# Performance work log

Hardware: AMD Instinct MI355X
Metric: run time of the kernel (lower is better)

Reference implementation:

```python
import jax, jax.numpy as jnp
import numpy as np

N = 8192
HID = 256
NCLS = 5
K = 10  # adj_parameter
IN_DIMS = [1000, 1000, 503]


def _leaky(x):
    return jnp.where(x >= 0, x, 0.25 * x)


def _batchnorm(x, g, b):
    # training-mode BatchNorm1d with batch stats (biased var), eps=1e-5
    mu = jnp.mean(x, axis=0)
    var = jnp.mean((x - mu) ** 2, axis=0)
    return (x - mu) * jax.lax.rsqrt(var + 1e-5) * g + b


def _build_adj(feat):
    # cosine similarity, per-row top-(K+1) (top-1 is self, diag=1), scatter,
    # add identity, L1 row-normalize. Vectorized equivalent of the torch loop.
    norm = jnp.maximum(jnp.linalg.norm(feat, axis=1, keepdims=True), 1e-12)
    fn = feat / norm
    sim = fn @ fn.T                                  # [N, N]
    vals, idx = jax.lax.top_k(sim, K + 1)            # [N, K+1]
    rows = jnp.arange(sim.shape[0])[:, None]
    adj = jnp.zeros_like(sim).at[rows, idx[:, 1:]].set(vals[:, 1:])
    adj = adj + jnp.eye(sim.shape[0], dtype=sim.dtype)
    rs = jnp.maximum(jnp.sum(jnp.abs(adj), axis=1, keepdims=True), 1e-12)
    return adj / rs


def setup_inputs() -> dict:
    key = jax.random.key(0)
    ks = jax.random.split(key, 24)
    d = {}
    d['x1'] = jax.random.normal(ks[0], (N, IN_DIMS[0]), jnp.float32)
    d['x2'] = jax.random.normal(ks[1], (N, IN_DIMS[1]), jnp.float32)
    d['x3'] = jax.random.normal(ks[2], (N, IN_DIMS[2]), jnp.float32)
    def xavier(k, shape):
        fan_in, fan_out = shape[-2], shape[-1]
        std = np.sqrt(2.0 / (fan_in + fan_out))
        return jax.random.normal(k, shape, jnp.float32) * std
    d['enc_W1'] = xavier(ks[3], (IN_DIMS[0], HID))
    d['enc_W2'] = xavier(ks[4], (IN_DIMS[1], HID))
    d['enc_W3'] = xavier(ks[5], (IN_DIMS[2], HID))
    d['enc_b'] = jnp.zeros((3, HID), jnp.float32)
    d['bn_g'] = jnp.ones((3, HID), jnp.float32)
    d['bn_b'] = jnp.zeros((3, HID), jnp.float32)
    d['gc1_W'] = xavier(ks[6], (3, HID, HID))
    d['gc1_b'] = jnp.zeros((3, HID), jnp.float32)
    d['gc2_W'] = xavier(ks[7], (3, HID, HID))
    d['gc2_b'] = jnp.zeros((3, HID), jnp.float32)
    d['clf_W'] = xavier(ks[8], (3, HID, NCLS))
    d['clf_b'] = jnp.zeros((3, NCLS), jnp.float32)
    d['attn'] = xavier(ks[9], (3, 1))[:, 0]
    d['f1_W'] = xavier(ks[10], (NCLS, 128))
    d['f1_b'] = jnp.zeros((128,), jnp.float32)
    d['f2_W'] = xavier(ks[11], (128, NCLS))
    d['f2_b'] = jnp.zeros((NCLS,), jnp.float32)
    return d


def reference(x1, x2, x3, enc_W1, enc_W2, enc_W3, enc_b, bn_g, bn_b,
              gc1_W, gc1_b, gc2_W, gc2_b, clf_W, clf_b,
              attn, f1_W, f1_b, f2_W, f2_b):
    xs = [x1, x2, x3]
    enc_Ws = [enc_W1, enc_W2, enc_W3]
    logits_list = []
    for i in range(3):
        # modal encoder: Linear -> ReLU -> BatchNorm (dropout off, eval)
        feat = jax.nn.relu(xs[i] @ enc_Ws[i] + enc_b[i])
        feat = _batchnorm(feat, bn_g[i], bn_b[i])
        adj = _build_adj(feat)
        # SimpleGCN: two GraphConvolution layers with leaky_relu(0.25)
        h = _leaky(adj @ (feat @ gc1_W[i]) + gc1_b[i])
        h = _leaky(adj @ (h @ gc2_W[i]) + gc2_b[i])
        logits_list.append(h @ clf_W[i] + clf_b[i])
    # SimpleVCDN fusion
    w = jax.nn.softmax(attn)
    fused = sum(w[i] * jax.nn.sigmoid(logits_list[i]) for i in range(3))
    out = _leaky(fused @ f1_W + f1_b) @ f2_W + f2_b
    return out
```

## Files before the change

### kernel.cpp

```cpp
#include <hip/hip_runtime.h>
#include <cfloat>
#include <cstdint>
#include <cstddef>

#define NROWS 8192
#define HID 256
#define NCLS 5
#define TOPK 10
#define CAP 256
#define TM 128
#define TN 128
#define BK 32
#define BKS 64

typedef __bf16 bf16x8 __attribute__((ext_vector_type(8)));
typedef float f32x4 __attribute__((ext_vector_type(4)));

__device__ inline ushort f2bf(float x) {
  unsigned u = __float_as_uint(x);
  unsigned r = (u + 0x7fffu + ((u >> 16) & 1u)) >> 16;
  return (ushort)r;
}
__device__ inline float bf2f(ushort b) { return __uint_as_float(((unsigned)b) << 16); }

__device__ __forceinline__ void load_lds16(const void* g, void* l) {
  __builtin_amdgcn_global_load_lds(
      (const __attribute__((address_space(1))) void*)g,
      (__attribute__((address_space(3))) void*)l, 16, 0, 0);
}

__global__ __launch_bounds__(256) void packAB_kernel(const float* __restrict__ X0,
    const float* __restrict__ X1, const float* __restrict__ X2,
    const float* __restrict__ W0, const float* __restrict__ W1,
    const float* __restrict__ W2, ushort* __restrict__ Ah, ushort* __restrict__ Al,
    ushort* __restrict__ Bh, ushort* __restrict__ Bl,
    int D0, int D1, int D2, int Kp0, int Kp1, int Kp2,
    size_t aOff0, size_t aOff1, size_t aOff2,
    size_t wOff0, size_t wOff1, size_t wOff2) {
  const int z = blockIdx.y;
  const float* X = (z == 0) ? X0 : (z == 1) ? X1 : X2;
  const float* W = (z == 0) ? W0 : (z == 1) ? W1 : W2;
  const int D = (z == 0) ? D0 : (z == 1) ? D1 : D2;
  const int Kp = (z == 0) ? Kp0 : (z == 1) ? Kp1 : Kp2;
  const size_t aOff = (z == 0) ? aOff0 : (z == 1) ? aOff1 : aOff2;
  const size_t wOff = (z == 0) ? wOff0 : (z == 1) ? wOff1 : wOff2;
  const int ksh = 31 - __clz(Kp);
  const int id = blockIdx.x * 256 + threadIdx.x;
  const int atotal = NROWS << ksh;
  if (id >= atotal + (HID << ksh)) return;
  if (id < atotal) {
    const int k = id & (Kp - 1);
    const int r = id >> ksh;
    const float x = (k < D) ? X[(size_t)r * D + k] : 0.f;
    const ushort h = f2bf(x);
    Ah[aOff + id] = h;
    Al[aOff + id] = f2bf(x - bf2f(h));
  } else {
    const int id2 = id - atotal;
    const int k = id2 & (Kp - 1);
    const int n = id2 >> ksh;
    const float x = (k < D) ? W[(size_t)k * HID + n] : 0.f;
    const ushort h = f2bf(x);
    Bh[wOff + id2] = h;
    Bl[wOff + id2] = f2bf(x - bf2f(h));
  }
}

__global__ __launch_bounds__(256) void packW_kernel(const float* __restrict__ W,
    ushort* __restrict__ Bh, ushort* __restrict__ Bl) {
  const int z = blockIdx.y;
  const int id = blockIdx.x * 256 + threadIdx.x;
  const int k = id >> 8, n = id & 255;
  const size_t wz = (size_t)z * HID * HID;
  const float x = W[wz + (size_t)k * HID + n];
  const ushort h = f2bf(x);
  Bh[wz + (size_t)n * HID + k] = h;
  Bl[wz + (size_t)n * HID + k] = f2bf(x - bf2f(h));
}

#define STAGE_LIMB(B, K0)                              \
    load_lds16(Ah + a0 + (K0), &AsH[B][p0 * 8]);       \
    load_lds16(Ah + a1 + (K0), &AsH[B][p1 * 8]);       \
    load_lds16(Al + a0 + (K0), &AsL[B][p0 * 8]);       \
    load_lds16(Al + a1 + (K0), &AsL[B][p1 * 8]);       \
    load_lds16(Bh + b0 + (K0), &BsH[B][p0 * 8]);       \
    load_lds16(Bh + b1 + (K0), &BsH[B][p1 * 8]);       \
    load_lds16(Bl + b0 + (K0), &BsL[B][p0 * 8]);       \
    load_lds16(Bl + b1 + (K0), &BsL[B][p1 * 8]);

template<bool BIAS, int ACT>
__global__ __launch_bounds__(256) void limbgemm_kernel(const ushort* __restrict__ Ah,
    const ushort* __restrict__ Al, const ushort* __restrict__ Bh,
    const ushort* __restrict__ Bl, const float* __restrict__ bias,
    float* __restrict__ C, int Kp0, int Kp1, int Kp2,
    size_t aOff0, size_t aOff1, size_t aOff2,
    size_t bOff0, size_t bOff1, size_t bOff2) {
  __shared__ ushort AsH[2][TM * BK], AsL[2][TM * BK], BsH[2][TM * BK], BsL[2][TM * BK];
  const int z = blockIdx.y;
  const int Kp = (z == 0) ? Kp0 : (z == 1) ? Kp1 : Kp2;
  const size_t aO = (z == 0) ? aOff0 : (z == 1) ? aOff1 : aOff2;
  const size_t bO = (z == 0) ? bOff0 : (z == 1) ? bOff1 : bOff2;
  Ah += aO; Al += aO; Bh += bO; Bl += bO;
  C += (size_t)z * NROWS * HID;
  const int tid = threadIdx.x;
  const int wave = tid >> 6, lane = tid & 63;
  const int bid = blockIdx.x;
  const int xcd = bid & 7, slot = bid >> 3;
  const int bxi = slot & 1;
  const int byi = xcd * 8 + (slot >> 1);
  const int bm = byi * TM, bn = bxi * 128;
  const int wr = (wave >> 1) * 64, wc = (wave & 1) * 64;

  f32x4 acc[4][4];
  const f32x4 zero = {0.f, 0.f, 0.f, 0.f};
  #pragma unroll
  for (int i = 0; i < 4; ++i)
    #pragma unroll
    for (int j = 0; j < 4; ++j) acc[i][j] = zero;

  const int p0 = tid, p1 = tid + 256;
  const int r0 = p0 >> 2, kl0 = (p0 & 3) ^ ((r0 & 3) ^ ((r0 >> 2) & 1));
  const int r1 = p1 >> 2, kl1 = (p1 & 3) ^ ((r1 & 3) ^ ((r1 >> 2) & 1));
  const size_t a0 = (size_t)(bm + r0) * Kp + kl0 * 8;
  const size_t a1 = (size_t)(bm + r1) * Kp + kl1 * 8;
  const size_t b0 = (size_t)(bn + r0) * Kp + kl0 * 8;
  const size_t b1 = (size_t)(bn + r1) * Kp + kl1 * 8;

  STAGE_LIMB(0, 0)
  __syncthreads();
  int cur = 0;
  for (int k0 = 0; k0 < Kp; k0 += BK) {
    if (k0 + BK < Kp) {
      STAGE_LIMB(cur ^ 1, k0 + BK)
    }
    bf16x8 ah[4], al[4], bh[4], bl[4];
    const int kg = lane >> 4;
    #pragma unroll
    for (int f = 0; f < 4; ++f) {
      const int m = wr + f * 16 + (lane & 15);
      const int sa = m * 4 + (kg ^ (m & 3) ^ ((m >> 2) & 1));
      ah[f] = *(const bf16x8*)&AsH[cur][sa * 8];
      al[f] = *(const bf16x8*)&AsL[cur][sa * 8];
      const int n = wc + f * 16 + (lane & 15);
      const int sb = n * 4 + (kg ^ (n & 3) ^ ((n >> 2) & 1));
      bh[f] = *(const bf16x8*)&BsH[cur][sb * 8];
      bl[f] = *(const bf16x8*)&BsL[cur][sb * 8];
    }
    #pragma unroll
    for (int fr = 0; fr < 4; ++fr)
      #pragma unroll
      for (int fc = 0; fc < 4; ++fc) {
        acc[fr][fc] = __builtin_amdgcn_mfma_f32_16x16x32_bf16(ah[fr], bh[fc], acc[fr][fc], 0, 0, 0);
        acc[fr][fc] = __builtin_amdgcn_mfma_f32_16x16x32_bf16(ah[fr], bl[fc], acc[fr][fc], 0, 0, 0);
        acc[fr][fc] = __builtin_amdgcn_mfma_f32_16x16x32_bf16(al[fr], bh[fc], acc[fr][fc], 0, 0, 0);
      }
    __syncthreads();
    cur ^= 1;
  }
  const int cq = lane >> 4, cc = lane & 15;
  #pragma unroll
  for (int fr = 0; fr < 4; ++fr) {
    #pragma unroll
    for (int fc = 0; fc < 4; ++fc) {
      const int rb = bm + wr + fr * 16 + cq * 4;
      const int col = bn + wc + fc * 16 + cc;
      const float bb = BIAS ? bias[z * HID + col] : 0.f;
      float* cp = C + (size_t)rb * HID + col;
      #pragma unroll
      for (int e = 0; e < 4; ++e) {
        float v = acc[fr][fc][e] + bb;
        if (ACT == 1) v = fmaxf(v, 0.f);
        cp[(size_t)e * HID] = v;
      }
    }
  }
}

__global__ __launch_bounds__(256) void bn_stats_kernel(const float* __restrict__ F,
    float* __restrict__ ps, float* __restrict__ ps2) {
  const int z = blockIdx.y;
  const int b = blockIdx.x, t = threadIdx.x;
  float s = 0.f, s2 = 0.f;
  const float* p = F + (size_t)z * NROWS * HID + (size_t)b * 128 * HID + t;
  for (int r = 0; r < 128; ++r) {
    const float v = p[(size_t)r * HID];
    s += v; s2 += v * v;
  }
  ps[(size_t)z * 64 * HID + b * HID + t] = s;
  ps2[(size_t)z * 64 * HID + b * HID + t] = s2;
}

__global__ __launch_bounds__(256) void bn_finalize_kernel(const float* __restrict__ ps,
    const float* __restrict__ ps2, const float* __restrict__ g,
    const float* __restrict__ b, float* __restrict__ scale, float* __restrict__ shift) {
  const int z = blockIdx.x;
  const int t = threadIdx.x;
  float s = 0.f, s2 = 0.f;
  for (int i = 0; i < 64; ++i) {
    s += ps[(size_t)z * 64 * HID + i * HID + t];
    s2 += ps2[(size_t)z * 64 * HID + i * HID + t];
  }
  const float mu = s / (float)NROWS;
  const float var = s2 / (float)NROWS - mu * mu;
  const float rstd = rsqrtf(var + 1e-5f);
  const float sc = rstd * g[z * HID + t];
  scale[z * HID + t] = sc;
  shift[z * HID + t] = b[z * HID + t] - mu * sc;
}

__global__ __launch_bounds__(256) void bn_rownorm_kernel(const float* __restrict__ F,
    const float* __restrict__ scale, const float* __restrict__ shift,
    float* __restrict__ FN, ushort* __restrict__ Ph,
    ushort* __restrict__ Fh, ushort* __restrict__ Fl) {
  const int z = blockIdx.y;
  const int r = blockIdx.x, t = threadIdx.x;
  const size_t zb = (size_t)z * NROWS * HID;
  const float f = F[zb + (size_t)r * HID + t] * scale[z * HID + t] + shift[z * HID + t];
  __shared__ float sh[256];
  sh[t] = f * f;
  __syncthreads();
  for (int st = 128; st > 0; st >>= 1) {
    if (t < st) sh[t] += sh[t + st];
    __syncthreads();
  }
  const float inv = 1.0f / fmaxf(sqrtf(sh[0]), 1e-12f);
  const float fn = f * inv;
  const size_t o = zb + (size_t)r * HID + t;
  FN[o] = fn;
  Ph[o] = f2bf(fn);
  const ushort h = f2bf(f);
  Fh[o] = h;
  Fl[o] = f2bf(f - bf2f(h));
}

template<int PASS>
__global__ __launch_bounds__(512) void simtile_kernel(const ushort* __restrict__ P,
    float* __restrict__ M, const float* __restrict__ tauv,
    int* __restrict__ gcnt, int* __restrict__ gidx) {
  const int tlin = blockIdx.x;
  int bx = (int)((sqrtf(8.0f * (float)tlin + 1.0f) - 1.0f) * 0.5f);
  while ((bx + 1) * (bx + 2) / 2 <= tlin) ++bx;
  while (bx * (bx + 1) / 2 > tlin) --bx;
  const int by = tlin - bx * (bx + 1) / 2;
  const int z = blockIdx.y;
  P += (size_t)z * NROWS * HID;
  if (PASS == 0) M += (size_t)z * NROWS * 64;
  else {
    tauv += (size_t)z * NROWS;
    gcnt += (size_t)z * NROWS;
    gidx += (size_t)z * NROWS * CAP;
  }
  const bool offdiag = (bx != by);
  __shared__ ushort As[2][TM * BKS];
  __shared__ ushort Bs[2][TN * BKS];
  __shared__ float Ml[2][TM];
  __shared__ float MlC[4][TN];
  __shared__ float taulA[TM];
  __shared__ float taulB[TN];
  const int tid = threadIdx.x;
  const int wave = tid >> 6, lane = tid & 63;
  const int bm = by * TM;
  const int bn = bx * TN;
  const int wr = (wave >> 1) * 32;
  const int wc = (wave & 1) * 64;

  if (PASS == 1) {
    if (tid < TM) taulA[tid] = tauv[bm + tid];
    else if (tid < TM + TN) taulB[tid - TM] = tauv[bn + (tid - TM)];
  }

  const ushort* pa[2];
  const ushort* pb[2];
  #pragma unroll
  for (int j = 0; j < 2; ++j) {
    const int s = tid + j * 512;
    const int m = s >> 3;
    const int kg = (s & 7) ^ (m & 7);
    pa[j] = P + (size_t)(bm + m) * HID + kg * 8;
    pb[j] = P + (size_t)(bn + m) * HID + kg * 8;
  }

  f32x4 acc[2][4];
  const f32x4 zero = {0.f, 0.f, 0.f, 0.f};
  #pragma unroll
  for (int i = 0; i < 2; ++i)
    #pragma unroll
    for (int j = 0; j < 4; ++j) acc[i][j] = zero;

  #pragma unroll
  for (int j = 0; j < 2; ++j) {
    load_lds16(pa[j], &As[0][(tid + j * 512) * 8]);
    load_lds16(pb[j], &Bs[0][(tid + j * 512) * 8]);
  }
  __syncthreads();
  int cur = 0;
  for (int k0 = 0; k0 < HID; k0 += BKS) {
    if (k0 + BKS < HID) {
      #pragma unroll
      for (int j = 0; j < 2; ++j) {
        load_lds16(pa[j] + k0 + BKS, &As[cur ^ 1][(tid + j * 512) * 8]);
        load_lds16(pb[j] + k0 + BKS, &Bs[cur ^ 1][(tid + j * 512) * 8]);
      }
    }
    #pragma unroll
    for (int h = 0; h < 2; ++h) {
      const int kgb = h * 4 + (lane >> 4);
      bf16x8 af[2], bfv[4];
      #pragma unroll
      for (int f = 0; f < 2; ++f) {
        const int m = wr + f * 16 + (lane & 15);
        const int sa = m * 8 + (kgb ^ (m & 7));
        af[f] = *(const bf16x8*)&As[cur][sa * 8];
      }
      #pragma unroll
      for (int f = 0; f < 4; ++f) {
        const int n = wc + f * 16 + (lane & 15);
        const int sb = n * 8 + (kgb ^ (n & 7));
        bfv[f] = *(const bf16x8*)&Bs[cur][sb * 8];
      }
      #pragma unroll
      for (int fr = 0; fr < 2; ++fr)
        #pragma unroll
        for (int fc = 0; fc < 4; ++fc)
          acc[fr][fc] = __builtin_amdgcn_mfma_f32_16x16x32_bf16(af[fr], bfv[fc], acc[fr][fc], 0, 0, 0);
    }
    __syncthreads();
    cur ^= 1;
  }

  const int cq = lane >> 4, cc = lane & 15;
  if (PASS == 0) {
    #pragma unroll
    for (int fr = 0; fr < 2; ++fr) {
      #pragma unroll
      for (int e = 0; e < 4; ++e) {
        const int lrow = wr + fr * 16 + cq * 4 + e;
        const int grow = bm + lrow;
        float mx = -FLT_MAX;
        #pragma unroll
        for (int fc = 0; fc < 4; ++fc) {
          const int col = bn + wc + fc * 16 + cc;
          mx = fmaxf(mx, (col == grow) ? -FLT_MAX : acc[fr][fc][e]);
        }
        #pragma unroll
        for (int s = 1; s < 16; s <<= 1) mx = fmaxf(mx, __shfl_xor(mx, s));
        if (cc == 0) Ml[wave & 1][lrow] = mx;
      }
    }
    if (offdiag) {
      #pragma unroll
      for (int fc = 0; fc < 4; ++fc) {
        float mx = -FLT_MAX;
        #pragma unroll
        for (int fr = 0; fr < 2; ++fr)
          #pragma unroll
          for (int e = 0; e < 4; ++e) mx = fmaxf(mx, acc[fr][fc][e]);
        mx = fmaxf(mx, __shfl_xor(mx, 16));
        mx = fmaxf(mx, __shfl_xor(mx, 32));
        if (cq == 0) MlC[wave >> 1][wc + fc * 16 + cc] = mx;
      }
    }
    __syncthreads();
    if (tid < TM) M[(size_t)(bm + tid) * 64 + bx] = fmaxf(Ml[0][tid], Ml[1][tid]);
    if (offdiag && tid < TN) {
      const float mx = fmaxf(fmaxf(MlC[0][tid], MlC[1][tid]),
                             fmaxf(MlC[2][tid], MlC[3][tid]));
      M[(size_t)(bn + tid) * 64 + by] = mx;
    }
  } else {
    __syncthreads();
    #pragma unroll
    for (int fr = 0; fr < 2; ++fr) {
      #pragma unroll
      for (int e = 0; e < 4; ++e) {
        const int lrow = wr + fr * 16 + cq * 4 + e;
        const int grow = bm + lrow;
        const float tA = taulA[lrow];
        #pragma unroll
        for (int fc = 0; fc < 4; ++fc) {
          const int lcol = wc + fc * 16 + cc;
          const int gcol = bn + lcol;
          const float v = acc[fr][fc][e];
          if (gcol != grow && v >= tA) {
            const int pos = atomicAdd(&gcnt[grow], 1);
            if (pos < CAP) gidx[(size_t)grow * CAP + pos] = gcol;
          }
          if (offdiag && v >= taulB[lcol]) {
            const int pos = atomicAdd(&gcnt[gcol], 1);
            if (pos < CAP) gidx[(size_t)gcol * CAP + pos] = grow;
          }
        }
      }
    }
  }
}

__global__ __launch_bounds__(256) void tau_kernel(const float* __restrict__ M,
    float* __restrict__ tauv, int* __restrict__ gcnt) {
  const int z = blockIdx.y;
  const int wave = threadIdx.x >> 6, lane = threadIdx.x & 63;
  const int row = blockIdx.x * 4 + wave;
  float cur = M[(size_t)z * NROWS * 64 + (size_t)row * 64 + lane];
  float tau = cur;
  #pragma unroll
  for (int sel = 0; sel < 16; ++sel) {
    float bv = cur;
    int bl = lane;
    #pragma unroll
    for (int s = 1; s < 64; s <<= 1) {
      const float ov = __shfl_xor(bv, s);
      const int ol = __shfl_xor(bl, s);
      if (ov > bv || (ov == bv && ol < bl)) { bv = ov; bl = ol; }
    }
    tau = bv;
    if (lane == bl) cur = -FLT_MAX;
  }
  if (lane == 0) {
    tauv[(size_t)z * NROWS + row] = tau;
    gcnt[(size_t)z * NROWS + row] = 0;
  }
}

__global__ __launch_bounds__(256) void refine_kernel(const int* __restrict__ gcnt,
    const int* __restrict__ gidx, const float* __restrict__ FN,
    int* __restrict__ nidx, float* __restrict__ nval, float* __restrict__ dinv) {
  const int z = blockIdx.y;
  gcnt += (size_t)z * NROWS;
  gidx += (size_t)z * NROWS * CAP;
  FN += (size_t)z * NROWS * HID;
  nidx += (size_t)z * NROWS * TOPK;
  nval += (size_t)z * NROWS * TOPK;
  dinv += (size_t)z * NROWS;
  const int wave = threadIdx.x >> 6, lane = threadIdx.x & 63;
  const int row = blockIdx.x * 4 + wave;
  const int cnt = min(gcnt[row], CAP);
  __shared__ float fnrow[4][HID];
  __shared__ float ev[4][CAP];
  ((float4*)fnrow[wave])[lane] = ((const float4*)(FN + (size_t)row * HID))[lane];
  __syncthreads();
  const int c = lane >> 2, q4 = lane & 3;
  for (int b0 = 0; b0 < cnt; b0 += 16) {
    const int ci = b0 + c;
    const int cand = (ci < cnt) ? gidx[(size_t)row * CAP + ci] : 0;
    float s = 0.f;
    const float* fc = FN + (size_t)cand * HID + q4 * 64;
    const float* fr = fnrow[wave] + q4 * 64;
    #pragma unroll 8
    for (int k = 0; k < 64; ++k) s += fr[k] * fc[k];
    s += __shfl_xor(s, 1);
    s += __shfl_xor(s, 2);
    if (q4 == 0 && ci < cnt) ev[wave][ci] = s;
  }
  __syncthreads();
  float outv[TOPK];
  int outi[TOPK];
  float sum = 1.0f;
  #pragma unroll
  for (int sel = 0; sel < TOPK; ++sel) {
    float bv = -FLT_MAX;
    int bp = 0;
    #pragma unroll
    for (int j = 0; j < 4; ++j) {
      const int p = lane + j * 64;
      if (p < cnt) {
        const float v = ev[wave][p];
        if (v > bv) { bv = v; bp = p; }
      }
    }
    #pragma unroll
    for (int s = 1; s < 64; s <<= 1) {
      const float ov = __shfl_xor(bv, s);
      const int op = __shfl_xor(bp, s);
      if (ov > bv || (ov == bv && op < bp)) { bv = ov; bp = op; }
    }
    outv[sel] = bv;
    outi[sel] = bp;
    sum += fabsf(bv);
    if (lane == 0) ev[wave][bp] = -FLT_MAX;
  }
  if (lane == 0) {
    const float inv = 1.0f / fmaxf(sum, 1e-12f);
    dinv[row] = inv;
    #pragma unroll
    for (int sel = 0; sel < TOPK; ++sel) {
      nval[row * TOPK + sel] = outv[sel] * inv;
      nidx[row * TOPK + sel] = gidx[(size_t)row * CAP + outi[sel]];
    }
  }
}

template<int EMIT>
__global__ __launch_bounds__(256) void spmm_kernel(const float* __restrict__ T,
    const int* __restrict__ nidx, const float* __restrict__ nval,
    const float* __restrict__ dinv, const float* __restrict__ bias,
    ushort* __restrict__ Hh, ushort* __restrict__ Hl,
    const float* __restrict__ clfW, const float* __restrict__ clfb,
    float* __restrict__ L) {
  const int z = blockIdx.y;
  const size_t zb = (size_t)z * NROWS * HID;
  T += zb;
  nidx += (size_t)z * NROWS * TOPK;
  nval += (size_t)z * NROWS * TOPK;
  dinv += (size_t)z * NROWS;
  const int r = blockIdx.x, c = threadIdx.x;
  float acc = dinv[r] * T[(size_t)r * HID + c];
  #pragma unroll
  for (int n = 0; n < TOPK; ++n) {
    acc += nval[r * TOPK + n] * T[(size_t)nidx[r * TOPK + n] * HID + c];
  }
  acc += bias[z * HID + c];
  const float v = acc >= 0.f ? acc : 0.25f * acc;
  if (EMIT == 1) {
    const size_t o = zb + (size_t)r * HID + c;
    const ushort h = f2bf(v);
    Hh[o] = h;
    Hl[o] = f2bf(v - bf2f(h));
  } else {
    __shared__ float wsum[4][NCLS];
    const int wave = c >> 6, lane = c & 63;
    const float* wrow = clfW + (size_t)z * HID * NCLS + (size_t)c * NCLS;
    #pragma unroll
    for (int cls = 0; cls < NCLS; ++cls) {
      float p = v * wrow[cls];
      #pragma unroll
      for (int s = 1; s < 64; s <<= 1) p += __shfl_xor(p, s);
      if (lane == 0) wsum[wave][cls] = p;
    }
    __syncthreads();
    if (c < NCLS) {
      const float lg = clfb[z * NCLS + c] + wsum[0][c] + wsum[1][c] + wsum[2][c] + wsum[3][c];
      L[(size_t)z * NROWS * NCLS + (size_t)r * NCLS + c] = lg;
    }
  }
}

__global__ __launch_bounds__(256) void fuse_kernel(const float* __restrict__ L,
    const float* __restrict__ attn, float* __restrict__ fused) {
  const int id = blockIdx.x * 256 + threadIdx.x;
  if (id >= NROWS * NCLS) return;
  const float a0 = attn[0], a1 = attn[1], a2 = attn[2];
  const float m = fmaxf(a0, fmaxf(a1, a2));
  const float e0 = expf(a0 - m), e1 = expf(a1 - m), e2 = expf(a2 - m);
  const float inv = 1.0f / (e0 + e1 + e2);
  const float l0 = L[id];
  const float l1 = L[NROWS * NCLS + id];
  const float l2 = L[2 * NROWS * NCLS + id];
  const float s0 = 1.0f / (1.0f + expf(-l0));
  const float s1 = 1.0f / (1.0f + expf(-l1));
  const float s2 = 1.0f / (1.0f + expf(-l2));
  fused[id] = (e0 * s0 + e1 * s1 + e2 * s2) * inv;
}

__global__ __launch_bounds__(128) void head_kernel(const float* __restrict__ fused,
    const float* __restrict__ W1, const float* __restrict__ b1,
    const float* __restrict__ W2, const float* __restrict__ b2,
    float* __restrict__ out) {
  const int r = blockIdx.x, t = threadIdx.x;
  __shared__ float f[NCLS];
  __shared__ float hh[128];
  if (t < NCLS) f[t] = fused[r * NCLS + t];
  __syncthreads();
  float s = b1[t];
  #pragma unroll
  for (int k = 0; k < NCLS; ++k) s += f[k] * W1[k * 128 + t];
  hh[t] = s >= 0.f ? s : 0.25f * s;
  __syncthreads();
  if (t < NCLS) {
    float o = b2[t];
    for (int k = 0; k < 128; ++k) o += hh[k] * W2[k * NCLS + t];
    out[r * NCLS + t] = o;
  }
}

extern "C" void kernel_launch(void* const* d_in, const int* in_sizes, int n_in,
                              void* d_out, int out_size, void* d_ws, size_t ws_size,
                              hipStream_t stream) {
  const float* x0 = (const float*)d_in[0];
  const float* x1 = (const float*)d_in[1];
  const float* x2 = (const float*)d_in[2];
  const float* eW0 = (const float*)d_in[3];
  const float* eW1 = (const float*)d_in[4];
  const float* eW2 = (const float*)d_in[5];
  const float* enc_b = (const float*)d_in[6];
  const float* bn_g  = (const float*)d_in[7];
  const float* bn_b  = (const float*)d_in[8];
  const float* gc1W  = (const float*)d_in[9];
  const float* gc1b  = (const float*)d_in[10];
  const float* gc2W  = (const float*)d_in[11];
  const float* gc2b  = (const float*)d_in[12];
  const float* clfW  = (const float*)d_in[13];
  const float* clfb  = (const float*)d_in[14];
  const float* attn  = (const float*)d_in[15];
  const float* f1W   = (const float*)d_in[16];
  const float* f1b   = (const float*)d_in[17];
  const float* f2W   = (const float*)d_in[18];
  const float* f2b   = (const float*)d_in[19];
  float* out = (float*)d_out;

  int Kp[3];
  for (int m = 0; m < 3; ++m) {
    const int D = in_sizes[m] / NROWS;
    int k = 256;
    while (k < D) k <<= 1;
    Kp[m] = k;
  }
  const size_t KpSum = (size_t)Kp[0] + Kp[1] + Kp[2];
  const int D0 = in_sizes[0] / NROWS, D1 = in_sizes[1] / NROWS, D2 = in_sizes[2] / NROWS;

  const size_t NH = (size_t)NROWS * HID;
  float* ws = (float*)d_ws;
  float* A = ws;
  float* C = A;
  float* nval = A + 3 * NH;
  int*   nidx = (int*)(nval + (size_t)3 * NROWS * TOPK);
  float* dinv = (float*)(nidx + (size_t)3 * NROWS * TOPK);
  float* logits = dinv + 3 * NROWS;
  float* fused = logits + (size_t)3 * NROWS * NCLS;
  float* ps    = fused + (size_t)NROWS * NCLS;
  float* ps2   = ps + 3 * 64 * HID;
  float* scale = ps2 + 3 * 64 * HID;
  float* shift = scale + 3 * HID;
  float* M     = shift + 3 * HID;
  float* tauv  = M + (size_t)3 * NROWS * 64;
  int*   gcnt  = (int*)(tauv + 3 * NROWS);
  int*   gidx  = gcnt + 3 * NROWS;
  ushort* WhG = (ushort*)(gidx + (size_t)3 * NROWS * CAP);
  ushort* WlG = WhG + (size_t)3 * HID * HID;
  ushort* WhE = WlG + (size_t)3 * HID * HID;
  ushort* WlE = WhE + (size_t)HID * KpSum;
  char* u3 = (char*)(WlE + (size_t)HID * KpSum);
  float* FN = (float*)u3;
  ushort* Ph = (ushort*)(FN + 3 * NH);
  ushort* Fh = Ph + 3 * NH;
  ushort* Fl = Fh + 3 * NH;
  ushort* Hh = Fl + 3 * NH;
  ushort* Hl = Hh + 3 * NH;
  ushort* AhE = (ushort*)u3;
  ushort* AlE = AhE + (size_t)NROWS * KpSum;

  const size_t aOff0 = 0, aOff1 = (size_t)NROWS * Kp[0],
               aOff2 = (size_t)NROWS * (Kp[0] + Kp[1]);
  const size_t wOff0 = 0, wOff1 = (size_t)HID * Kp[0],
               wOff2 = (size_t)HID * (Kp[0] + Kp[1]);

  const dim3 blk(256);
  packAB_kernel<<<dim3(((NROWS + HID) * 1024) / 256, 3), blk, 0, stream>>>(
      x0, x1, x2, eW0, eW1, eW2, AhE, AlE, WhE, WlE,
      D0, D1, D2, Kp[0], Kp[1], Kp[2], aOff0, aOff1, aOff2, wOff0, wOff1, wOff2);
  limbgemm_kernel<true, 1><<<dim3(128, 3), blk, 0, stream>>>(
      AhE, AlE, WhE, WlE, enc_b, A, Kp[0], Kp[1], Kp[2],
      aOff0, aOff1, aOff2, wOff0, wOff1, wOff2);
  bn_stats_kernel<<<dim3(64, 3), blk, 0, stream>>>(A, ps, ps2);
  bn_finalize_kernel<<<3, blk, 0, stream>>>(ps, ps2, bn_g, bn_b, scale, shift);
  bn_rownorm_kernel<<<dim3(NROWS, 3), blk, 0, stream>>>(A, scale, shift, FN, Ph, Fh, Fl);
  simtile_kernel<0><<<dim3(2080, 3), dim3(512), 0, stream>>>(Ph, M, nullptr, nullptr, nullptr);
  tau_kernel<<<dim3(NROWS / 4, 3), blk, 0, stream>>>(M, tauv, gcnt);
  simtile_kernel<1><<<dim3(2080, 3), dim3(512), 0, stream>>>(Ph, nullptr, tauv, gcnt, gidx);
  refine_kernel<<<dim3(NROWS / 4, 3), blk, 0, stream>>>(gcnt, gidx, FN, nidx, nval, dinv);
  packW_kernel<<<dim3(256, 3), blk, 0, stream>>>(gc1W, WhG, WlG);
  limbgemm_kernel<false, 0><<<dim3(128, 3), blk, 0, stream>>>(
      Fh, Fl, WhG, WlG, nullptr, C, HID, HID, HID,
      0, NH, 2 * NH, 0, (size_t)HID * HID, (size_t)2 * HID * HID);
  spmm_kernel<1><<<dim3(NROWS, 3), blk, 0, stream>>>(C, nidx, nval, dinv, gc1b,
                                                     Hh, Hl, nullptr, nullptr, nullptr);
  packW_kernel<<<dim3(256, 3), blk, 0, stream>>>(gc2W, WhG, WlG);
  limbgemm_kernel<false, 0><<<dim3(128, 3), blk, 0, stream>>>(
      Hh, Hl, WhG, WlG, nullptr, C, HID, HID, HID,
      0, NH, 2 * NH, 0, (size_t)HID * HID, (size_t)2 * HID * HID);
  spmm_kernel<0><<<dim3(NROWS, 3), blk, 0, stream>>>(C, nidx, nval, dinv, gc2b,
                                                     nullptr, nullptr, clfW, clfb, logits);
  fuse_kernel<<<(NROWS * NCLS + 255) / 256, blk, 0, stream>>>(logits, attn, fused);
  head_kernel<<<NROWS, dim3(128), 0, stream>>>(fused, f1W, f1b, f2W, f2b, out);
}
```

Baseline: 813.6 us.

## Load full K slab in two halves and swizzle triangular tile order in simtile

The similarity-tile kernel now stages K in two 128-wide halves. Both halves are issued up front, and the rolling double-buffered 64-wide loop is gone, leaving one barrier mid-compute instead of one per step. The linear block index is also remapped into 8 interleaved groups of 260 triangular tiles, so concurrently running blocks touch nearby rows for better cache reuse. LDS per block roughly doubles, to about 128KB, which likely limits the kernel to one 512-thread block per CU and reduces latency hiding.

Measured after the change: 984.3 us. 1.21x slower.

```diff
diff --git a/kernel.cpp b/kernel.cpp
--- a/kernel.cpp
+++ b/kernel.cpp
@@ -11,7 +11,6 @@
 #define TM 128
 #define TN 128
 #define BK 32
-#define BKS 64
 
 typedef __bf16 bf16x8 __attribute__((ext_vector_type(8)));
 typedef float f32x4 __attribute__((ext_vector_type(4)));
@@ -237,7 +236,8 @@
 __global__ __launch_bounds__(512) void simtile_kernel(const ushort* __restrict__ P,
     float* __restrict__ M, const float* __restrict__ tauv,
     int* __restrict__ gcnt, int* __restrict__ gidx) {
-  const int tlin = blockIdx.x;
+  const int orig = blockIdx.x;
+  const int tlin = (orig & 7) * 260 + (orig >> 3);
   int bx = (int)((sqrtf(8.0f * (float)tlin + 1.0f) - 1.0f) * 0.5f);
   while ((bx + 1) * (bx + 2) / 2 <= tlin) ++bx;
   while (bx * (bx + 1) / 2 > tlin) --bx;
@@ -251,8 +251,8 @@
     gidx += (size_t)z * NROWS * CAP;
   }
   const bool offdiag = (bx != by);
-  __shared__ ushort As[2][TM * BKS];
-  __shared__ ushort Bs[2][TN * BKS];
+  __shared__ ushort As[2][TM * 128];
+  __shared__ ushort Bs[2][TN * 128];
   __shared__ float Ml[2][TM];
   __shared__ float MlC[4][TN];
   __shared__ float taulA[TM];
@@ -269,13 +269,14 @@
     else if (tid < TM + TN) taulB[tid - TM] = tauv[bn + (tid - TM)];
   }
 
-  const ushort* pa[2];
-  const ushort* pb[2];
-  #pragma unroll
-  for (int j = 0; j < 2; ++j) {
+  const ushort* pa[4];
+  const ushort* pb[4];
+  #pragma unroll
+  for (int j = 0; j < 4; ++j) {
     const int s = tid + j * 512;
-    const int m = s >> 3;
-    const int kg = (s & 7) ^ (m & 7);
+    const int m = s >> 4;
+    const int kgp = s & 15;
+    const int kg = (kgp & 8) | ((kgp & 7) ^ (m & 7));
     pa[j] = P + (size_t)(bm + m) * HID + kg * 8;
     pb[j] = P + (size_t)(bn + m) * HID + kg * 8;
   }
@@ -288,35 +289,33 @@
     for (int j = 0; j < 4; ++j) acc[i][j] = zero;
 
   #pragma unroll
-  for (int j = 0; j < 2; ++j) {
+  for (int j = 0; j < 4; ++j) {
     load_lds16(pa[j], &As[0][(tid + j * 512) * 8]);
     load_lds16(pb[j], &Bs[0][(tid + j * 512) * 8]);
   }
   __syncthreads();
-  int cur = 0;
-  for (int k0 = 0; k0 < HID; k0 += BKS) {
-    if (k0 + BKS < HID) {
-      #pragma unroll
-      for (int j = 0; j < 2; ++j) {
-        load_lds16(pa[j] + k0 + BKS, &As[cur ^ 1][(tid + j * 512) * 8]);
-        load_lds16(pb[j] + k0 + BKS, &Bs[cur ^ 1][(tid + j * 512) * 8]);
-      }
-    }
-    #pragma unroll
-    for (int h = 0; h < 2; ++h) {
-      const int kgb = h * 4 + (lane >> 4);
+  #pragma unroll
+  for (int j = 0; j < 4; ++j) {
+    load_lds16(pa[j] + 128, &As[1][(tid + j * 512) * 8]);
+    load_lds16(pb[j] + 128, &Bs[1][(tid + j * 512) * 8]);
+  }
+  #pragma unroll
+  for (int half = 0; half < 2; ++half) {
+    #pragma unroll
+    for (int ks = 0; ks < 4; ++ks) {
+      const int kc = ks * 4 + (lane >> 4);
       bf16x8 af[2], bfv[4];
       #pragma unroll
       for (int f = 0; f < 2; ++f) {
         const int m = wr + f * 16 + (lane & 15);
-        const int sa = m * 8 + (kgb ^ (m & 7));
-        af[f] = *(const bf16x8*)&As[cur][sa * 8];
+        const int ph = (kc & 8) | ((kc & 7) ^ (m & 7));
+        af[f] = *(const bf16x8*)&As[half][m * 128 + ph * 8];
       }
       #pragma unroll
       for (int f = 0; f < 4; ++f) {
         const int n = wc + f * 16 + (lane & 15);
-        const int sb = n * 8 + (kgb ^ (n & 7));
-        bfv[f] = *(const bf16x8*)&Bs[cur][sb * 8];
+        const int ph = (kc & 8) | ((kc & 7) ^ (n & 7));
+        bfv[f] = *(const bf16x8*)&Bs[half][n * 128 + ph * 8];
       }
       #pragma unroll
       for (int fr = 0; fr < 2; ++fr)
@@ -324,8 +323,7 @@
         for (int fc = 0; fc < 4; ++fc)
           acc[fr][fc] = __builtin_amdgcn_mfma_f32_16x16x32_bf16(af[fr], bfv[fc], acc[fr][fc], 0, 0, 0);
     }
-    __syncthreads();
-    cur ^= 1;
+    if (half == 0) __syncthreads();
   }
 
   const int cq = lane >> 4, cc = lane & 15;
```
